# Kernel optimization log

Hardware: AMD Instinct MI355X
Metric: run time of the kernel (lower is better)

The kernel has to match this reference:

```python
import jax, jax.numpy as jnp
import numpy as np


def setup_inputs() -> dict:
    key = jax.random.key(0)
    ks = jax.random.split(key, 16)
    H, F, W, Hh, C = 8, 256, 96, 96, 64
    inp = {
        "X": jax.random.normal(ks[0], (F, W, Hh), jnp.float32),
        "WQ_task": jax.random.uniform(ks[1], (H, F, 1, 1), jnp.float32),
        "BQ_task": jax.random.uniform(ks[2], (H, F, 1, 1), jnp.float32),
        "WK_task": jax.random.uniform(ks[3], (F, 1, 1), jnp.float32),
        "BK_task": jax.random.uniform(ks[4], (F, 1, 1), jnp.float32),
        "WV_task": jax.random.uniform(ks[5], (C, 1, 1), jnp.float32),
        "BV_task": jax.random.uniform(ks[6], (C, 1, 1), jnp.float32),
        "WQ_t_minus_1": jax.random.uniform(ks[7], (H, F, 1, 1), jnp.float32),
        "WQ_x": jax.random.uniform(ks[8], (1, F, 1, 1), jnp.float32),
        "BQ": jax.random.uniform(ks[9], (H, F, 1, 1), jnp.float32),
        "WK_x": jax.random.uniform(ks[10], (F, 1, 1), jnp.float32),
        "BK": jax.random.uniform(ks[11], (F, 1, 1), jnp.float32),
        "prev_Q": jax.random.normal(ks[12], (H, F, W, Hh), jnp.float32),
        "Vconv_w": jax.random.normal(ks[13], (C, F, 3, 3), jnp.float32) * 0.02,
        "Vconv_b": jnp.zeros((C,), jnp.float32),
    }
    return inp


def reference(X, WQ_task, BQ_task, WK_task, BK_task, WV_task, BV_task,
              WQ_t_minus_1, WQ_x, BQ, WK_x, BK, prev_Q, Vconv_w, Vconv_b):
    F, W, Hh = X.shape
    C = Vconv_w.shape[0]
    rX = X[None]  # (1, F, W, Hh)

    # Q: (n_heads, F, W, Hh); K: (F, W, Hh)
    Q = WQ_task * (WQ_t_minus_1 * prev_Q + WQ_x * rX + BQ) + BQ_task
    K = WK_task * (WK_x * X + BK) + BK_task

    # Original: similarity = sum over [head, feature] of Q[n,f,w,h] * K[f,v,u]
    # (K is broadcast over heads) == dot(Q.sum(heads), K) over features.
    Qs = Q.sum(axis=0)  # (F, W, Hh)
    sim = jnp.einsum('fwh,fvu->whvu', Qs, K).reshape(W, Hh, W * Hh)
    attn = jax.nn.softmax(sim, axis=-1)  # softmax over flattened key positions

    # V: 3x3 same conv F -> C, then task affine
    V = jax.lax.conv_general_dilated(
        rX, Vconv_w, window_strides=(1, 1), padding='SAME',
        dimension_numbers=('NCHW', 'OIHW', 'NCHW'))
    V = (WV_task * (V[0] + Vconv_b[:, None, None]) + BV_task).reshape(C, W * Hh)

    # out[c, w, h] = sum_k attn[w, h, k] * V[c, k]
    out = jnp.einsum('whk,ck->cwh', attn, V)
    return out
```

## Files before the change

### kernel.cpp

```cpp
#include <hip/hip_runtime.h>
#include <hip/hip_fp16.h>

#define S 9216
#define F 256
#define W 96
#define HH 96
#define C 64
#define NH 8
#define KSPLIT 16
#define KV_PER_SPLIT (S / KSPLIT)
#define KTILE 32
#define NKT (KV_PER_SPLIT / KTILE)
#define TILE_H8 1280

typedef _Float16 half8 __attribute__((ext_vector_type(8)));
typedef float floatx4 __attribute__((ext_vector_type(4)));


__global__ __launch_bounds__(256) void rowmean_kernel(
    const float* __restrict__ prevQ, const float* __restrict__ Xg,
    float* __restrict__ pqmean, float* __restrict__ xmean) {
  int row = blockIdx.x;
  const float4* src = (const float4*)((row < 2048) ? (prevQ + (size_t)row * S)
                                                   : (Xg + (size_t)(row - 2048) * S));
  float s = 0.f;
  #pragma unroll
  for (int j = 0; j < 9; j++) {
    float4 v = src[j * 256 + threadIdx.x];
    s += v.x + v.y + v.z + v.w;
  }
  __shared__ float red[256];
  red[threadIdx.x] = s;
  __syncthreads();
  for (int off = 128; off > 0; off >>= 1) {
    if ((int)threadIdx.x < off) red[threadIdx.x] += red[threadIdx.x + off];
    __syncthreads();
  }
  if (threadIdx.x == 0) {
    float m = red[0] * (1.f / (float)S);
    if (row < 2048) pqmean[row] = m; else xmean[row - 2048] = m;
  }
}

__global__ __launch_bounds__(256) void coef_kernel(
    const float* __restrict__ WQ_task, const float* __restrict__ BQ_task,
    const float* __restrict__ WK_task, const float* __restrict__ BK_task,
    const float* __restrict__ WQ_tm1, const float* __restrict__ WQ_x,
    const float* __restrict__ BQ, const float* __restrict__ WK_x,
    const float* __restrict__ BK, const float* __restrict__ pqmean,
    const float* __restrict__ xmean,
    float* __restrict__ qscale, float* __restrict__ c1, float* __restrict__ c0,
    float* __restrict__ kw, float* __restrict__ kb,
    float* __restrict__ qbar, float* __restrict__ kbar) {
  int f = threadIdx.x;
  float sumW = 0.f, sc0 = 0.f, qb = 0.f;
  for (int n = 0; n < NH; n++) {
    float wq = WQ_task[n * F + f];
    float qs = wq * WQ_tm1[n * F + f];
    qscale[f * NH + n] = qs;
    sumW += wq;
    sc0 += wq * BQ[n * F + f] + BQ_task[n * F + f];
    qb += qs * pqmean[n * F + f];
  }
  float c1v = WQ_x[f] * sumW;
  c1[f] = c1v; c0[f] = sc0;
  float kwv = WK_task[f] * WK_x[f];
  float kbv = WK_task[f] * BK[f] + BK_task[f];
  kw[f] = kwv; kb[f] = kbv;
  qbar[f] = qb + c1v * xmean[f] + sc0;
  kbar[f] = kwv * xmean[f] + kbv;
}

__global__ __launch_bounds__(256) void prep_kernel(
    const float* __restrict__ Xg, const float* __restrict__ prevQ,
    const float* __restrict__ qscale, const float* __restrict__ c1,
    const float* __restrict__ c0, const float* __restrict__ kw,
    const float* __restrict__ kb, const float* __restrict__ qbar,
    const float* __restrict__ kbar,
    _Float16* __restrict__ Qf, _Float16* __restrict__ Kf,
    float* __restrict__ rowK) {
  __shared__ float qt[32][33];
  __shared__ float kt[32][33];
  __shared__ float rk[8][32];
  int tx = threadIdx.x & 31, ty = threadIdx.x >> 5;
  int s0 = blockIdx.x * 32, f0 = blockIdx.y * 32;
  int s = s0 + tx;
  float rkacc = 0.f;
  for (int fi = ty; fi < 32; fi += 8) {
    int f = f0 + fi;
    float x = Xg[(size_t)f * S + s];
    float q = c1[f] * x + c0[f];
    #pragma unroll
    for (int n = 0; n < NH; n++)
      q += qscale[f * NH + n] * prevQ[((size_t)n * F + f) * S + s];
    q -= qbar[f];
    float k = kw[f] * x + kb[f] - kbar[f];
    qt[fi][tx] = q;
    kt[fi][tx] = k;
    rkacc += qbar[f] * k;
  }
  rk[ty][tx] = rkacc;
  __syncthreads();
  {
    int t = threadIdx.x;
    int isK = t >> 7;
    int tt = t & 127;
    int s_sub = tt >> 2, lw = tt & 3;
    half8 h;
    #pragma unroll
    for (int jj = 0; jj < 8; jj++) {
      float v = isK ? kt[lw * 8 + jj][s_sub] : qt[lw * 8 + jj][s_sub];
      h[jj] = (_Float16)v;
    }
    size_t fi = (size_t)((s0 + s_sub) >> 4) * 8 + (f0 >> 5);
    int lane = (s_sub & 15) + 16 * lw;
    half8* dst = (half8*)(isK ? Kf : Qf);
    dst[fi * 64 + lane] = h;
  }
  if (ty == 0) {
    float t = 0.f;
    #pragma unroll
    for (int i = 0; i < 8; i++) t += rk[i][tx];
    atomicAdd(&rowK[s], t);
  }
}

__global__ __launch_bounds__(256) void conv_kernel(
    const float* __restrict__ Xg, const float* __restrict__ Wc,
    const float* __restrict__ bias, const float* __restrict__ WV_task,
    const float* __restrict__ BV_task, _Float16* __restrict__ Vf) {
  __shared__ float wlds[4 * 2304];
  int c0 = blockIdx.y * 4;
  for (int i = threadIdx.x; i < 4 * 2304; i += 256)
    wlds[i] = Wc[(size_t)c0 * 2304 + i];
  __syncthreads();
  int p = blockIdx.x * 256 + threadIdx.x;
  int w = p / HH, h = p % HH;
  float acc0 = 0.f, acc1 = 0.f, acc2 = 0.f, acc3 = 0.f;
  for (int f = 0; f < F; f++) {
    const float* xp = Xg + (size_t)f * S;
    float xv[9];
    #pragma unroll
    for (int ky = 0; ky < 3; ky++) {
      int ww = w + ky - 1;
      #pragma unroll
      for (int kx = 0; kx < 3; kx++) {
        int hh = h + kx - 1;
        xv[ky * 3 + kx] = (ww >= 0 && ww < W && hh >= 0 && hh < HH)
                              ? xp[ww * HH + hh] : 0.f;
      }
    }
    const float* wl = wlds + f * 9;
    #pragma unroll
    for (int t = 0; t < 9; t++) {
      float x = xv[t];
      acc0 += x * wl[t];
      acc1 += x * wl[2304 + t];
      acc2 += x * wl[2 * 2304 + t];
      acc3 += x * wl[3 * 2304 + t];
    }
  }
  float accs[4] = {acc0, acc1, acc2, acc3};
  int k = p;
  #pragma unroll
  for (int cc = 0; cc < 4; cc++) {
    int c = c0 + cc;
    float v = WV_task[c] * (accs[cc] + bias[c]) + BV_task[c];
    size_t idx = (((size_t)(k >> 5) * 4 + (c >> 4)) * 64 +
                  ((c & 15) + 16 * ((k & 31) >> 3))) * 8 + (k & 7);
    Vf[idx] = (_Float16)v;
  }
}

__global__ __launch_bounds__(256, 3) void flash_kernel(
    const _Float16* __restrict__ Qf, const _Float16* __restrict__ Kf,
    const _Float16* __restrict__ Vf, const float* __restrict__ rowK,
    _Float16* __restrict__ out_part, float* __restrict__ m_part,
    float* __restrict__ l_part) {
  int qt = blockIdx.x, sp = blockIdx.y;
  int wave = threadIdx.x >> 6, lane = threadIdx.x & 63;
  int tid = threadIdx.x;
  int lr = lane & 15, lhi = lane >> 4;
  __shared__ __align__(16) half8 kv[2][TILE_H8];
  __shared__ __align__(16) _Float16 plds[4][16][40];

  half8 qfrag[2][8];
  #pragma unroll
  for (int qs = 0; qs < 2; qs++) {
    size_t t16 = (size_t)(qt * 8 + wave * 2 + qs) * 8;
    #pragma unroll
    for (int ch = 0; ch < 8; ch++)
      qfrag[qs][ch] = ((const half8*)Qf)[(t16 + ch) * 64 + lane];
  }

  floatx4 oacc[2][4] = {};
  float m_run[2][4], l_run[2][4];
  #pragma unroll
  for (int qs = 0; qs < 2; qs++)
    #pragma unroll
    for (int j = 0; j < 4; j++) { m_run[qs][j] = -1e30f; l_run[qs][j] = 0.f; }

  {
    int k0 = sp * KV_PER_SPLIT;
    const half8* ks = (const half8*)Kf + (size_t)(k0 >> 4) * 512;
    const half8* vs = (const half8*)Vf + (size_t)(k0 >> 5) * 256;
    #pragma unroll
    for (int u = 0; u < 5; u++) {
      int idx = u * 256 + tid;
      kv[0][idx] = (idx < 1024) ? ks[idx] : vs[idx - 1024];
    }
  }

  int cur = 0;
  for (int kt = 0; kt < NKT; kt++) {
    int k0 = sp * KV_PER_SPLIT + kt * KTILE;
    half8 stg[5];
    if (kt + 1 < NKT) {
      const half8* ks = (const half8*)Kf + (size_t)((k0 + KTILE) >> 4) * 512;
      const half8* vs = (const half8*)Vf + (size_t)((k0 + KTILE) >> 5) * 256;
      #pragma unroll
      for (int u = 0; u < 5; u++) {
        int idx = u * 256 + tid;
        stg[u] = (idx < 1024) ? ks[idx] : vs[idx - 1024];
      }
    }
    __builtin_amdgcn_sched_barrier(0);
    __syncthreads();

    float rk4[2];
    #pragma unroll
    for (int ks = 0; ks < 2; ks++) rk4[ks] = rowK[k0 + ks * 16 + lr];

    floatx4 sacc[2][2] = {};
    #pragma unroll
    for (int ch = 0; ch < 8; ch++) {
      #pragma unroll
      for (int ks = 0; ks < 2; ks++) {
        half8 kf = kv[cur][(ks * 8 + ch) * 64 + lane];
        sacc[0][ks] = __builtin_amdgcn_mfma_f32_16x16x32_f16(qfrag[0][ch], kf,
                                                             sacc[0][ks], 0, 0, 0);
        sacc[1][ks] = __builtin_amdgcn_mfma_f32_16x16x32_f16(qfrag[1][ch], kf,
                                                             sacc[1][ks], 0, 0, 0);
      }
    }

    #pragma unroll
    for (int qs = 0; qs < 2; qs++) {
      float tmax[4];
      #pragma unroll
      for (int j = 0; j < 4; j++) tmax[j] = -1e30f;
      #pragma unroll
      for (int ks = 0; ks < 2; ks++) {
        #pragma unroll
        for (int j = 0; j < 4; j++) {
          sacc[qs][ks][j] += rk4[ks];
          tmax[j] = fmaxf(tmax[j], sacc[qs][ks][j]);
        }
      }
      #pragma unroll
      for (int off = 1; off < 16; off <<= 1)
        #pragma unroll
        for (int j = 0; j < 4; j++)
          tmax[j] = fmaxf(tmax[j], __shfl_xor(tmax[j], off, 64));

      float ef[4], rsum[4];
      #pragma unroll
      for (int j = 0; j < 4; j++) {
        float mn = fmaxf(m_run[qs][j], tmax[j]);
        ef[j] = __expf(m_run[qs][j] - mn);
        m_run[qs][j] = mn;
        rsum[j] = 0.f;
      }
      #pragma unroll
      for (int ks = 0; ks < 2; ks++) {
        #pragma unroll
        for (int j = 0; j < 4; j++) {
          float p = __expf(sacc[qs][ks][j] - m_run[qs][j]);
          rsum[j] += p;
          plds[wave][lhi * 4 + j][ks * 16 + lr] = (_Float16)p;
        }
      }
      #pragma unroll
      for (int off = 1; off < 16; off <<= 1)
        #pragma unroll
        for (int j = 0; j < 4; j++) rsum[j] += __shfl_xor(rsum[j], off, 64);
      #pragma unroll
      for (int j = 0; j < 4; j++)
        l_run[qs][j] = l_run[qs][j] * ef[j] + rsum[j];
      #pragma unroll
      for (int cs = 0; cs < 4; cs++)
        #pragma unroll
        for (int j = 0; j < 4; j++) oacc[qs][cs][j] *= ef[j];

      half8 pfrag = *(const half8*)(&plds[wave][lr][lhi * 8]);
      #pragma unroll
      for (int cs = 0; cs < 4; cs++) {
        half8 vfrag = kv[cur][1024 + cs * 64 + lane];
        oacc[qs][cs] = __builtin_amdgcn_mfma_f32_16x16x32_f16(pfrag, vfrag,
                                                              oacc[qs][cs], 0, 0, 0);
      }
    }

    if (kt + 1 < NKT) {
      #pragma unroll
      for (int u = 0; u < 5; u++) kv[cur ^ 1][u * 256 + tid] = stg[u];
    }
    cur ^= 1;
  }

  #pragma unroll
  for (int qs = 0; qs < 2; qs++) {
    size_t base = (size_t)sp * S + qt * 128 + wave * 32 + qs * 16;
    #pragma unroll
    for (int cs = 0; cs < 4; cs++)
      #pragma unroll
      for (int j = 0; j < 4; j++)
        out_part[(base + lhi * 4 + j) * C + cs * 16 + lr] =
            (_Float16)oacc[qs][cs][j];
    if (lr == 0) {
      #pragma unroll
      for (int j = 0; j < 4; j++) {
        m_part[base + lhi * 4 + j] = m_run[qs][j];
        l_part[base + lhi * 4 + j] = l_run[qs][j];
      }
    }
  }
}

__global__ __launch_bounds__(256) void combine_kernel(
    const _Float16* __restrict__ out_part, const float* __restrict__ m_part,
    const float* __restrict__ l_part, float* __restrict__ out) {
  int q = blockIdx.x * 4 + (threadIdx.x >> 6);
  int c = threadIdx.x & 63;
  float m = -1e30f;
  #pragma unroll
  for (int i = 0; i < KSPLIT; i++) m = fmaxf(m, m_part[(size_t)i * S + q]);
  float l = 0.f, acc = 0.f;
  #pragma unroll
  for (int i = 0; i < KSPLIT; i++) {
    float wgt = __expf(m_part[(size_t)i * S + q] - m);
    l += wgt * l_part[(size_t)i * S + q];
    acc += wgt * (float)out_part[((size_t)i * S + q) * C + c];
  }
  out[(size_t)c * S + q] = acc / l;
}

extern "C" void kernel_launch(void* const* d_in, const int* in_sizes, int n_in,
                              void* d_out, int out_size, void* d_ws,
                              size_t ws_size, hipStream_t stream) {
  const float* Xg      = (const float*)d_in[0];
  const float* WQ_task = (const float*)d_in[1];
  const float* BQ_task = (const float*)d_in[2];
  const float* WK_task = (const float*)d_in[3];
  const float* BK_task = (const float*)d_in[4];
  const float* WV_task = (const float*)d_in[5];
  const float* BV_task = (const float*)d_in[6];
  const float* WQ_tm1  = (const float*)d_in[7];
  const float* WQ_x    = (const float*)d_in[8];
  const float* BQ      = (const float*)d_in[9];
  const float* WK_x    = (const float*)d_in[10];
  const float* BK      = (const float*)d_in[11];
  const float* prevQ   = (const float*)d_in[12];
  const float* Wc      = (const float*)d_in[13];
  const float* bias    = (const float*)d_in[14];
  float* out = (float*)d_out;

  char* ws = (char*)d_ws;
  size_t off = 0;
  auto alloc = [&](size_t bytes) {
    void* p = ws + off;
    off += (bytes + 255) & ~(size_t)255;
    return p;
  };
  _Float16* Qf   = (_Float16*)alloc((size_t)S * F * 2);
  _Float16* Kf   = (_Float16*)alloc((size_t)S * F * 2);
  _Float16* Vf   = (_Float16*)alloc((size_t)C * S * 2);
  float* rowK    = (float*)alloc((size_t)S * 4);
  float* pqmean  = (float*)alloc(2048 * 4);
  float* xmean   = (float*)alloc(256 * 4);
  float* qscale  = (float*)alloc(256 * 8 * 4);
  float* c1      = (float*)alloc(256 * 4);
  float* c0      = (float*)alloc(256 * 4);
  float* kw      = (float*)alloc(256 * 4);
  float* kb      = (float*)alloc(256 * 4);
  float* qbar    = (float*)alloc(256 * 4);
  float* kbar    = (float*)alloc(256 * 4);
  _Float16* out_part = (_Float16*)alloc((size_t)KSPLIT * S * C * 2);
  float* m_part   = (float*)alloc((size_t)KSPLIT * S * 4);
  float* l_part   = (float*)alloc((size_t)KSPLIT * S * 4);

  hipMemsetAsync(rowK, 0, (size_t)S * 4, stream);

  rowmean_kernel<<<2304, 256, 0, stream>>>(prevQ, Xg, pqmean, xmean);
  coef_kernel<<<1, 256, 0, stream>>>(WQ_task, BQ_task, WK_task, BK_task,
                                     WQ_tm1, WQ_x, BQ, WK_x, BK, pqmean, xmean,
                                     qscale, c1, c0, kw, kb, qbar, kbar);
  prep_kernel<<<dim3(S / 32, F / 32), 256, 0, stream>>>(
      Xg, prevQ, qscale, c1, c0, kw, kb, qbar, kbar, Qf, Kf, rowK);
  conv_kernel<<<dim3(S / 256, C / 4), 256, 0, stream>>>(Xg, Wc, bias, WV_task,
                                                        BV_task, Vf);
  flash_kernel<<<dim3(S / 128, KSPLIT), 256, 0, stream>>>(
      Qf, Kf, Vf, rowK, out_part, m_part, l_part);
  combine_kernel<<<S / 4, 256, 0, stream>>>(out_part, m_part, l_part, out);
}
```

Measured before the change: 472.9 us.

## Compute softmax row sums via MFMA with ones vector, load V from global directly

Replaces the shuffle-reduction of softmax row sums with an extra MFMA against a ones column, which accumulates the sums in matrix-core registers. V fragments are now read straight from global memory into registers each tile instead of being staged through shared memory, which shrinks the LDS buffer. KSPLIT drops from 16 to 12 and launch bounds go up to 4 blocks per SIMD to raise occupancy. The direct V loads are not prefetched, so their latency may be exposed, and the P values are summed in fp16 form, which slightly changes precision.

```diff
diff --git a/kernel.cpp b/kernel.cpp
--- a/kernel.cpp
+++ b/kernel.cpp
@@ -7,11 +7,10 @@
 #define HH 96
 #define C 64
 #define NH 8
-#define KSPLIT 16
+#define KSPLIT 12
 #define KV_PER_SPLIT (S / KSPLIT)
 #define KTILE 32
 #define NKT (KV_PER_SPLIT / KTILE)
-#define TILE_H8 1280
 
 typedef _Float16 half8 __attribute__((ext_vector_type(8)));
 typedef float floatx4 __attribute__((ext_vector_type(4)));
@@ -172,7 +171,7 @@
   }
 }
 
-__global__ __launch_bounds__(256, 3) void flash_kernel(
+__global__ __launch_bounds__(256, 4) void flash_kernel(
     const _Float16* __restrict__ Qf, const _Float16* __restrict__ Kf,
     const _Float16* __restrict__ Vf, const float* __restrict__ rowK,
     _Float16* __restrict__ out_part, float* __restrict__ m_part,
@@ -181,8 +180,12 @@
   int wave = threadIdx.x >> 6, lane = threadIdx.x & 63;
   int tid = threadIdx.x;
   int lr = lane & 15, lhi = lane >> 4;
-  __shared__ __align__(16) half8 kv[2][TILE_H8];
+  __shared__ __align__(16) half8 kv[2][1024];
   __shared__ __align__(16) _Float16 plds[4][16][40];
+
+  half8 ones_b;
+  #pragma unroll
+  for (int j = 0; j < 8; j++) ones_b[j] = (_Float16)((lr == 0) ? 1.f : 0.f);
 
   half8 qfrag[2][8];
   #pragma unroll
@@ -194,42 +197,39 @@
   }
 
   floatx4 oacc[2][4] = {};
-  float m_run[2][4], l_run[2][4];
+  floatx4 lacc[2] = {};
+  float m_run[2][4];
   #pragma unroll
   for (int qs = 0; qs < 2; qs++)
     #pragma unroll
-    for (int j = 0; j < 4; j++) { m_run[qs][j] = -1e30f; l_run[qs][j] = 0.f; }
+    for (int j = 0; j < 4; j++) m_run[qs][j] = -1e30f;
 
   {
-    int k0 = sp * KV_PER_SPLIT;
-    const half8* ks = (const half8*)Kf + (size_t)(k0 >> 4) * 512;
-    const half8* vs = (const half8*)Vf + (size_t)(k0 >> 5) * 256;
-    #pragma unroll
-    for (int u = 0; u < 5; u++) {
-      int idx = u * 256 + tid;
-      kv[0][idx] = (idx < 1024) ? ks[idx] : vs[idx - 1024];
-    }
+    const half8* ks = (const half8*)Kf +
+                      (size_t)((sp * KV_PER_SPLIT) >> 4) * 512;
+    #pragma unroll
+    for (int u = 0; u < 4; u++) kv[0][u * 256 + tid] = ks[u * 256 + tid];
   }
 
   int cur = 0;
   for (int kt = 0; kt < NKT; kt++) {
     int k0 = sp * KV_PER_SPLIT + kt * KTILE;
-    half8 stg[5];
+    half8 stg[4];
     if (kt + 1 < NKT) {
       const half8* ks = (const half8*)Kf + (size_t)((k0 + KTILE) >> 4) * 512;
-      const half8* vs = (const half8*)Vf + (size_t)((k0 + KTILE) >> 5) * 256;
-      #pragma unroll
-      for (int u = 0; u < 5; u++) {
-        int idx = u * 256 + tid;
-        stg[u] = (idx < 1024) ? ks[idx] : vs[idx - 1024];
-      }
+      #pragma unroll
+      for (int u = 0; u < 4; u++) stg[u] = ks[u * 256 + tid];
     }
     __builtin_amdgcn_sched_barrier(0);
     __syncthreads();
 
-    float rk4[2];
-    #pragma unroll
-    for (int ks = 0; ks < 2; ks++) rk4[ks] = rowK[k0 + ks * 16 + lr];
+    const half8* vs = (const half8*)Vf + (size_t)(k0 >> 5) * 256;
+    half8 vf[4];
+    #pragma unroll
+    for (int cs = 0; cs < 4; cs++) vf[cs] = vs[cs * 64 + lane];
+    float rk2[2];
+    #pragma unroll
+    for (int ks = 0; ks < 2; ks++) rk2[ks] = rowK[k0 + ks * 16 + lr];
 
     floatx4 sacc[2][2] = {};
     #pragma unroll
@@ -253,7 +253,7 @@
       for (int ks = 0; ks < 2; ks++) {
         #pragma unroll
         for (int j = 0; j < 4; j++) {
-          sacc[qs][ks][j] += rk4[ks];
+          sacc[qs][ks][j] += rk2[ks];
           tmax[j] = fmaxf(tmax[j], sacc[qs][ks][j]);
         }
       }
@@ -263,47 +263,40 @@
         for (int j = 0; j < 4; j++)
           tmax[j] = fmaxf(tmax[j], __shfl_xor(tmax[j], off, 64));
 
-      float ef[4], rsum[4];
+      float ef[4];
       #pragma unroll
       for (int j = 0; j < 4; j++) {
         float mn = fmaxf(m_run[qs][j], tmax[j]);
         ef[j] = __expf(m_run[qs][j] - mn);
         m_run[qs][j] = mn;
-        rsum[j] = 0.f;
       }
       #pragma unroll
       for (int ks = 0; ks < 2; ks++) {
         #pragma unroll
         for (int j = 0; j < 4; j++) {
           float p = __expf(sacc[qs][ks][j] - m_run[qs][j]);
-          rsum[j] += p;
           plds[wave][lhi * 4 + j][ks * 16 + lr] = (_Float16)p;
         }
       }
       #pragma unroll
-      for (int off = 1; off < 16; off <<= 1)
+      for (int j = 0; j < 4; j++) {
         #pragma unroll
-        for (int j = 0; j < 4; j++) rsum[j] += __shfl_xor(rsum[j], off, 64);
-      #pragma unroll
-      for (int j = 0; j < 4; j++)
-        l_run[qs][j] = l_run[qs][j] * ef[j] + rsum[j];
+        for (int cs = 0; cs < 4; cs++) oacc[qs][cs][j] *= ef[j];
+        lacc[qs][j] *= ef[j];
+      }
+
+      half8 pfrag = *(const half8*)(&plds[wave][lr][lhi * 8]);
       #pragma unroll
       for (int cs = 0; cs < 4; cs++)
-        #pragma unroll
-        for (int j = 0; j < 4; j++) oacc[qs][cs][j] *= ef[j];
-
-      half8 pfrag = *(const half8*)(&plds[wave][lr][lhi * 8]);
-      #pragma unroll
-      for (int cs = 0; cs < 4; cs++) {
-        half8 vfrag = kv[cur][1024 + cs * 64 + lane];
-        oacc[qs][cs] = __builtin_amdgcn_mfma_f32_16x16x32_f16(pfrag, vfrag,
+        oacc[qs][cs] = __builtin_amdgcn_mfma_f32_16x16x32_f16(pfrag, vf[cs],
                                                               oacc[qs][cs], 0, 0, 0);
-      }
+      lacc[qs] = __builtin_amdgcn_mfma_f32_16x16x32_f16(pfrag, ones_b,
+                                                        lacc[qs], 0, 0, 0);
     }
 
     if (kt + 1 < NKT) {
       #pragma unroll
-      for (int u = 0; u < 5; u++) kv[cur ^ 1][u * 256 + tid] = stg[u];
+      for (int u = 0; u < 4; u++) kv[cur ^ 1][u * 256 + tid] = stg[u];
     }
     cur ^= 1;
   }
@@ -321,7 +314,7 @@
       #pragma unroll
       for (int j = 0; j < 4; j++) {
         m_part[base + lhi * 4 + j] = m_run[qs][j];
-        l_part[base + lhi * 4 + j] = l_run[qs][j];
+        l_part[base + lhi * 4 + j] = lacc[qs][j];
       }
     }
   }
```

After: 548.4 us. 16.0% more time.
